# Optimization experiments

Hardware: AMD Instinct MI355X
Metric: run time of the kernel (lower is better)

## Reference

```python
import jax, jax.numpy as jnp
import numpy as np

NUM_HEADS = 16
SIGMA_DATA = 1.0


def setup_inputs() -> dict:
    key = jax.random.key(0)
    ks = jax.random.split(key, 6)
    B, N, C = 4, 2048, 1024
    x = jax.random.normal(ks[0], (B, N, C), dtype=jnp.float32)
    t = jax.random.uniform(ks[1], (B,), dtype=jnp.float32)
    # Linear layers stored as (in, out) so y = x @ W + b
    Wqkv = jax.random.normal(ks[2], (C, 3 * C), dtype=jnp.float32) * (C ** -0.5)
    bqkv = jax.random.normal(ks[3], (3 * C,), dtype=jnp.float32) * 0.02
    Wproj = jax.random.normal(ks[4], (C, C), dtype=jnp.float32) * (C ** -0.5)
    bproj = jax.random.normal(ks[5], (C,), dtype=jnp.float32) * 0.02
    return {"x": x, "t": t, "Wqkv": Wqkv, "bqkv": bqkv, "Wproj": Wproj, "bproj": bproj}


def reference(x, t, Wqkv, bqkv, Wproj, bproj):
    B, N, C = x.shape
    H = NUM_HEADS
    Dh = C // H
    scale = Dh ** -0.5

    qkv = (x @ Wqkv + bqkv).reshape(B, N, 3, H, Dh)
    qkv = jnp.transpose(qkv, (2, 0, 3, 1, 4))
    q, k, v = qkv[0], qkv[1], qkv[2]

    # softmax attention
    scores = jnp.einsum("bhmd,bhnd->bhmn", q, k) * scale
    attn = jax.nn.softmax(scores, axis=-1)
    o = jnp.einsum("bhmn,bhnd->bhmd", attn, v)          # [B, H, N, Dh]
    o = jnp.transpose(o, (0, 2, 1, 3)).reshape(B, N, C)  # [B, N, C]

    # rCM skip coefficients; kernel launch collapses per-batch coeffs to their mean (scalar)
    sd2 = SIGMA_DATA ** 2
    c_skip = (sd2 / (t * t + sd2)).mean()
    c_out = (SIGMA_DATA * t / jnp.sqrt(sd2 + t * t)).mean()

    out = c_skip * x + c_out * o  # fused epilogue
    return out @ Wproj + bproj
```

## Files before the change

### kernel.cpp

```cpp
#include <hip/hip_runtime.h>


typedef unsigned short ushort_t;
typedef __bf16 bf16x8 __attribute__((ext_vector_type(8)));
typedef float f32x4 __attribute__((ext_vector_type(4)));

#define GAS __attribute__((address_space(1)))
#define LAS __attribute__((address_space(3)))

static __device__ __forceinline__ ushort_t f2bf(float f) {
  union { float f; unsigned int u; } v; v.f = f;
  unsigned int r = v.u + 0x7fffu + ((v.u >> 16) & 1u);
  return (ushort_t)(r >> 16);
}

static __device__ __forceinline__ void async16(const void* g, void* l) {
  __builtin_amdgcn_global_load_lds((const GAS unsigned int*)g,
                                   (LAS unsigned int*)l, 16, 0, 0);
}

__global__ __launch_bounds__(256) void prep_kernel(
    const float* __restrict__ x, ushort_t* __restrict__ Xbf,
    const float* __restrict__ Wqkv, ushort_t* __restrict__ WqkvT,
    const float* __restrict__ Wproj, ushort_t* __restrict__ WprojT) {
  __shared__ float tile[32][33];
  const int bid = (int)blockIdx.x, tid = threadIdx.x;
  if (bid < 8192) {
    int i = (bid * 256 + tid) * 4;
    float4 v = *(const float4*)(x + i);
    ushort4 o = make_ushort4(f2bf(v.x), f2bf(v.y), f2bf(v.z), f2bf(v.w));
    *(ushort4*)(Xbf + i) = o;
    return;
  }
  const float* in;
  ushort_t* out;
  int R, C, bx, by;
  if (bid < 11264) {
    int q = bid - 8192;
    by = q / 96; bx = q - by * 96;
    in = Wqkv; out = WqkvT; R = 1024; C = 3072;
  } else {
    int p = bid - 11264;
    bx = p & 31; by = p >> 5;
    in = Wproj; out = WprojT; R = 1024; C = 1024;
  }
  int bc = bx * 32, br = by * 32;
  int tx = tid & 31, ty = tid >> 5;
#pragma unroll
  for (int i = 0; i < 32; i += 8)
    tile[ty + i][tx] = in[(size_t)(br + ty + i) * C + bc + tx];
  __syncthreads();
#pragma unroll
  for (int i = 0; i < 32; i += 8)
    out[(size_t)(bc + ty + i) * R + br + tx] = f2bf(tile[tx][ty + i]);
}

static __device__ __forceinline__ void gemm128_core(
    const ushort_t* __restrict__ A, const ushort_t* __restrict__ Bt, int K,
    int m0, int n0, ushort_t* As, ushort_t* Bs, f32x4 acc[4][4]) {
  const int tid = threadIdx.x;
  const int wave = tid >> 6, lane = tid & 63;
  const int wm = (wave >> 1) * 64, wn = (wave & 1) * 64;
  const int lr = lane & 15, quad = lane >> 4;
  const int ch = ((quad + (lr >> 1)) & 3) * 8;
  for (int kb = 0; kb < K; kb += 32) {
#pragma unroll
    for (int i = 0; i < 2; ++i) {
      int c = (i * 4 + wave) * 64 + lane;
      int row = c >> 2;
      int cg = (((c & 3) - ((c >> 3) & 3)) & 3) * 8;
      async16(A + (size_t)(m0 + row) * K + kb + cg, As + (i * 4 + wave) * 512);
      async16(Bt + (size_t)(n0 + row) * K + kb + cg, Bs + (i * 4 + wave) * 512);
    }
    __syncthreads();
    bf16x8 af[4], bfr[4];
#pragma unroll
    for (int i = 0; i < 4; ++i) {
      af[i]  = *(const bf16x8*)(As + (wm + i * 16 + lr) * 32 + ch);
      bfr[i] = *(const bf16x8*)(Bs + (wn + i * 16 + lr) * 32 + ch);
    }
#pragma unroll
    for (int i = 0; i < 4; ++i)
#pragma unroll
      for (int j = 0; j < 4; ++j)
        acc[i][j] = __builtin_amdgcn_mfma_f32_16x16x32_bf16(af[i], bfr[j], acc[i][j], 0, 0, 0);
    __syncthreads();
  }
}

static __device__ __forceinline__ void grid_decode(int bid, int& m0, int& n0) {
  m0 = (((bid & 7) << 3) | ((bid >> 3) & 7)) << 7;
  n0 = (bid >> 6) << 7;
}

__global__ __launch_bounds__(256) void gemm_qkv_kernel(
    const ushort_t* __restrict__ Xbf, const ushort_t* __restrict__ Wt,
    const float* __restrict__ bqkv, ushort_t* __restrict__ Qb,
    ushort_t* __restrict__ Kb, ushort_t* __restrict__ Vb) {
  __shared__ __align__(16) ushort_t As[128 * 32];
  __shared__ __align__(16) ushort_t Bs[128 * 32];
  int m0, n0;
  grid_decode((int)blockIdx.x, m0, n0);
  f32x4 acc[4][4];
#pragma unroll
  for (int i = 0; i < 4; ++i)
#pragma unroll
    for (int j = 0; j < 4; ++j) acc[i][j] = f32x4{0.f, 0.f, 0.f, 0.f};
  gemm128_core(Xbf, Wt, 1024, m0, n0, As, Bs, acc);

  const int tid = threadIdx.x, wave = tid >> 6, lane = tid & 63;
  const int wm = (wave >> 1) * 64, wn = (wave & 1) * 64;
  const int col = lane & 15, quad = lane >> 4;
  const int b = m0 >> 11;
  const float C1 = 0.18033688011112042f;
#pragma unroll
  for (int j = 0; j < 4; ++j) {
    int jc = n0 + wn + j * 16 + col;
    float bj = bqkv[jc];
    int which = jc >> 10, rem = jc & 1023;
    int hh = rem >> 6, d = rem & 63;
    if (which == 2) {
      size_t vb2 = ((size_t)(b * 16 + hh) * 64 + d) * 2048;
#pragma unroll
      for (int i = 0; i < 4; ++i) {
        int nbase = (m0 + wm + i * 16 + quad * 4) & 2047;
        int npos = (nbase & ~31) | (((nbase >> 2) & 3) << 3) | (((nbase >> 4) & 1) << 2);
        ushort4 pk = make_ushort4(f2bf(acc[i][j][0] + bj), f2bf(acc[i][j][1] + bj),
                                  f2bf(acc[i][j][2] + bj), f2bf(acc[i][j][3] + bj));
        *(ushort4*)(Vb + vb2 + npos) = pk;
      }
    } else {
      ushort_t* dst = which == 0 ? Qb : Kb;
      float sc = which == 0 ? C1 : 1.0f;
      size_t base = ((size_t)(b * 16 + hh) * 2048) * 64 + d;
#pragma unroll
      for (int i = 0; i < 4; ++i)
#pragma unroll
        for (int r = 0; r < 4; ++r) {
          int nseq = (m0 + wm + i * 16 + quad * 4 + r) & 2047;
          dst[base + (size_t)nseq * 64] = f2bf((acc[i][j][r] + bj) * sc);
        }
    }
  }
}

__global__ __launch_bounds__(256) void gemm_out_kernel(
    const ushort_t* __restrict__ Hbf, const ushort_t* __restrict__ Wt,
    const float* __restrict__ bproj, float* __restrict__ out) {
  __shared__ __align__(16) ushort_t As[128 * 32];
  __shared__ __align__(16) ushort_t Bs[128 * 32];
  int m0, n0;
  grid_decode((int)blockIdx.x, m0, n0);
  f32x4 acc[4][4];
#pragma unroll
  for (int i = 0; i < 4; ++i)
#pragma unroll
    for (int j = 0; j < 4; ++j) acc[i][j] = f32x4{0.f, 0.f, 0.f, 0.f};
  gemm128_core(Hbf, Wt, 1024, m0, n0, As, Bs, acc);

  const int tid = threadIdx.x, wave = tid >> 6, lane = tid & 63;
  const int wm = (wave >> 1) * 64, wn = (wave & 1) * 64;
  const int col = lane & 15, quad = lane >> 4;
#pragma unroll
  for (int j = 0; j < 4; ++j) {
    int jc = n0 + wn + j * 16 + col;
    float bj = bproj[jc];
#pragma unroll
    for (int i = 0; i < 4; ++i)
#pragma unroll
      for (int r = 0; r < 4; ++r) {
        int m = m0 + wm + i * 16 + quad * 4 + r;
        out[(size_t)m * 1024 + jc] = acc[i][j][r] + bj;
      }
  }
}

__global__ __launch_bounds__(256, 4) void attn_kernel(
    const ushort_t* __restrict__ Qb, const ushort_t* __restrict__ Kb,
    const ushort_t* __restrict__ Vb, const float* __restrict__ x,
    const float* __restrict__ t, ushort_t* __restrict__ Hbf) {
  __shared__ __align__(16) ushort_t Ks[2][64 * 64];
  __shared__ __align__(16) ushort_t Vs[2][64 * 64];

  const int tid = threadIdx.x, w = tid >> 6, lane = tid & 63;
  const int m = lane & 15, q = lane >> 4;
  const int bid = (int)blockIdx.x;
  const int wg = (bid & 7) * 128 + (bid >> 3);
  const int bh = wg >> 4, rowbase = ((wg & 15) << 7) + w * 32;

  const ushort_t* Qg = Qb + ((size_t)bh * 2048 + rowbase) * 64;
  const ushort_t* Kg = Kb + (size_t)bh * 2048 * 64;
  const ushort_t* Vg = Vb + (size_t)bh * 64 * 2048;

  bf16x8 qf[2][2];
#pragma unroll
  for (int qt = 0; qt < 2; ++qt) {
    qf[qt][0] = *(const bf16x8*)(Qg + (qt * 16 + m) * 64 + q * 8);
    qf[qt][1] = *(const bf16x8*)(Qg + (qt * 16 + m) * 64 + 32 + q * 8);
  }

  auto stage = [&](int kt, int buf) {
#pragma unroll
    for (int i = 0; i < 2; ++i) {
      int f = i * 256 + tid;
      int r = f >> 3, g = (f & 7) ^ (r & 7);
      async16(Kg + (size_t)(kt * 64 + r) * 64 + g * 8,
              Ks[buf] + (size_t)(i * 256 + w * 64) * 8);
    }
#pragma unroll
    for (int i = 0; i < 2; ++i) {
      int f = i * 256 + tid;
      int d = f >> 3, g = (f & 7) ^ (d & 7);
      async16(Vg + (size_t)d * 2048 + kt * 64 + g * 8,
              Vs[buf] + (size_t)(i * 256 + w * 64) * 8);
    }
  };
  stage(0, 0);

  f32x4 oacc[2][4], lacc[2];
#pragma unroll
  for (int qt = 0; qt < 2; ++qt) {
    lacc[qt] = f32x4{0.f, 0.f, 0.f, 0.f};
#pragma unroll
    for (int dt = 0; dt < 4; ++dt) oacc[qt][dt] = f32x4{0.f, 0.f, 0.f, 0.f};
  }

  const float C2 = -23.083120654223414f;
  const f32x4 c2v = {C2, C2, C2, C2};
  const int mk = m & 7;
  union { bf16x8 v; unsigned int u[4]; } onesu;
#pragma unroll
  for (int h = 0; h < 4; ++h) onesu.u[h] = 0x3F803F80u;
  const bf16x8 ones = onesu.v;

#pragma unroll 2
  for (int kt = 0; kt < 32; ++kt) {
    const int cur = kt & 1;
    __syncthreads();
    if (kt < 31) stage(kt + 1, cur ^ 1);
    const ushort_t* K0 = Ks[cur];
    const ushort_t* V0 = Vs[cur];

#pragma unroll
    for (int p = 0; p < 2; ++p) {
      f32x4 st[2][2];
#pragma unroll
      for (int sh = 0; sh < 2; ++sh) {
        int s = p * 2 + sh;
        bf16x8 kf0 = *(const bf16x8*)(K0 + (s * 16 + m) * 64 + (q ^ mk) * 8);
        bf16x8 kf1 = *(const bf16x8*)(K0 + (s * 16 + m) * 64 + ((q + 4) ^ mk) * 8);
#pragma unroll
        for (int qt = 0; qt < 2; ++qt) {
          f32x4 a = __builtin_amdgcn_mfma_f32_16x16x32_bf16(kf0, qf[qt][0], c2v, 0, 0, 0);
          st[sh][qt] = __builtin_amdgcn_mfma_f32_16x16x32_bf16(kf1, qf[qt][1], a, 0, 0, 0);
        }
      }
      bf16x8 pf[2];
#pragma unroll
      for (int qt = 0; qt < 2; ++qt) {
        float pv[8];
#pragma unroll
        for (int sh = 0; sh < 2; ++sh)
#pragma unroll
          for (int rr = 0; rr < 4; ++rr)
            pv[sh * 4 + rr] = __builtin_amdgcn_exp2f(st[sh][qt][rr]);
        union { bf16x8 v; unsigned int u[4]; } pk;
#pragma unroll
        for (int h = 0; h < 4; ++h)
          pk.u[h] = __builtin_amdgcn_perm(__float_as_uint(pv[2 * h + 1]),
                                          __float_as_uint(pv[2 * h]), 0x07060302);
        pf[qt] = pk.v;
      }
#pragma unroll
      for (int dt = 0; dt < 4; ++dt) {
        bf16x8 vf = *(const bf16x8*)(V0 + (dt * 16 + m) * 64 + ((p * 4 + q) ^ mk) * 8);
#pragma unroll
        for (int qt = 0; qt < 2; ++qt)
          oacc[qt][dt] = __builtin_amdgcn_mfma_f32_16x16x32_bf16(vf, pf[qt], oacc[qt][dt], 0, 0, 0);
      }
#pragma unroll
      for (int qt = 0; qt < 2; ++qt)
        lacc[qt] = __builtin_amdgcn_mfma_f32_16x16x32_bf16(ones, pf[qt], lacc[qt], 0, 0, 0);
    }
  }

  float cs = 0.f, co = 0.f;
#pragma unroll
  for (int i = 0; i < 4; ++i) {
    float ti = t[i];
    float d = 1.f + ti * ti;
    cs += 1.f / d;
    co += ti / sqrtf(d);
  }
  cs *= 0.25f; co *= 0.25f;

  const int b = bh >> 4, hh = bh & 15;
#pragma unroll
  for (int qt = 0; qt < 2; ++qt) {
    float inv = co / lacc[qt][0];
    int nseq = rowbase + qt * 16 + m;
#pragma unroll
    for (int dt = 0; dt < 4; ++dt) {
      int c0 = hh * 64 + dt * 16 + q * 4;
      size_t midx = ((size_t)b * 2048 + nseq) * 1024 + c0;
      float4 xv = *(const float4*)(x + midx);
      ushort4 hv = make_ushort4(f2bf(cs * xv.x + oacc[qt][dt][0] * inv),
                                f2bf(cs * xv.y + oacc[qt][dt][1] * inv),
                                f2bf(cs * xv.z + oacc[qt][dt][2] * inv),
                                f2bf(cs * xv.w + oacc[qt][dt][3] * inv));
      *(ushort4*)(Hbf + midx) = hv;
    }
  }
}

extern "C" void kernel_launch(void* const* d_in, const int* in_sizes, int n_in,
                              void* d_out, int out_size, void* d_ws, size_t ws_size,
                              hipStream_t stream) {
  const float* x     = (const float*)d_in[0];
  const float* t     = (const float*)d_in[1];
  const float* Wqkv  = (const float*)d_in[2];
  const float* bqkv  = (const float*)d_in[3];
  const float* Wproj = (const float*)d_in[4];
  const float* bproj = (const float*)d_in[5];
  float* out = (float*)d_out;
  char* ws = (char*)d_ws;

  ushort_t* Xbf    = (ushort_t*)(ws + 256);
  ushort_t* WqkvT  = (ushort_t*)(ws + 256 + 16777216);
  ushort_t* WprojT = (ushort_t*)(ws + 256 + 16777216 + 6291456);
  ushort_t* Qb     = (ushort_t*)(ws + 256 + 16777216 + 6291456 + 2097152);
  ushort_t* Kb = Qb + 8388608;
  ushort_t* Vb = Kb + 8388608;
  ushort_t* Hb = Vb + 8388608;

  prep_kernel<<<12288, 256, 0, stream>>>(x, Xbf, Wqkv, WqkvT, Wproj, WprojT);
  gemm_qkv_kernel<<<1536, 256, 0, stream>>>(Xbf, WqkvT, bqkv, Qb, Kb, Vb);
  attn_kernel<<<1024, 256, 0, stream>>>(Qb, Kb, Vb, x, t, Hb);
  gemm_out_kernel<<<512, 256, 0, stream>>>(Hb, WprojT, bproj, out);
}
```

Before: 263.6 us.

## Double-buffer GEMM core with async LDS prefetch and 64-wide K tiles

Rewrites the shared 128x128 GEMM mainloop to use two LDS buffers, each holding a K-slice of 64 instead of 32. The next tile's global-to-LDS loads are issued while the current tile's MFMAs run, using explicit vmcnt waits and raw barriers in place of two __syncthreads per step. It also switches to an XOR swizzle over 8 chunks to avoid LDS bank conflicts. LDS use per block grows fourfold (to 64 KB), which may reduce occupancy, and the hand-placed waitcnt and barriers add correctness risk.

```diff
diff --git a/kernel.cpp b/kernel.cpp
--- a/kernel.cpp
+++ b/kernel.cpp
@@ -62,29 +62,54 @@
   const int wave = tid >> 6, lane = tid & 63;
   const int wm = (wave >> 1) * 64, wn = (wave & 1) * 64;
   const int lr = lane & 15, quad = lane >> 4;
-  const int ch = ((quad + (lr >> 1)) & 3) * 8;
-  for (int kb = 0; kb < K; kb += 32) {
-#pragma unroll
-    for (int i = 0; i < 2; ++i) {
-      int c = (i * 4 + wave) * 64 + lane;
-      int row = c >> 2;
-      int cg = (((c & 3) - ((c >> 3) & 3)) & 3) * 8;
-      async16(A + (size_t)(m0 + row) * K + kb + cg, As + (i * 4 + wave) * 512);
-      async16(Bt + (size_t)(n0 + row) * K + kb + cg, Bs + (i * 4 + wave) * 512);
-    }
-    __syncthreads();
-    bf16x8 af[4], bfr[4];
-#pragma unroll
-    for (int i = 0; i < 4; ++i) {
-      af[i]  = *(const bf16x8*)(As + (wm + i * 16 + lr) * 32 + ch);
-      bfr[i] = *(const bf16x8*)(Bs + (wn + i * 16 + lr) * 32 + ch);
-    }
+  const int lm = lr & 7;
+
+  auto stage = [&](int kb, int buf) {
+#pragma unroll
+    for (int u = 0; u < 4; ++u) {
+      int f = u * 256 + tid;
+      int r = f >> 3, g = (f & 7) ^ (r & 7);
+      async16(A + (size_t)(m0 + r) * K + kb + g * 8,
+              As + buf * 8192 + (u * 256 + wave * 64) * 8);
+      async16(Bt + (size_t)(n0 + r) * K + kb + g * 8,
+              Bs + buf * 8192 + (u * 256 + wave * 64) * 8);
+    }
+  };
+  stage(0, 0);
+  stage(64, 1);
+
+  const int nt = K >> 6;
+#pragma unroll 2
+  for (int t = 0; t < nt; ++t) {
+    const int cur = t & 1;
+    if (t + 1 < nt) asm volatile("s_waitcnt vmcnt(8)" ::: "memory");
+    else            asm volatile("s_waitcnt vmcnt(0)" ::: "memory");
+    __builtin_amdgcn_s_barrier();
+    __builtin_amdgcn_sched_barrier(0);
+    const ushort_t* As0 = As + cur * 8192;
+    const ushort_t* Bs0 = Bs + cur * 8192;
+    bf16x8 af[4][2], bfr[4][2];
 #pragma unroll
     for (int i = 0; i < 4; ++i)
 #pragma unroll
+      for (int ks = 0; ks < 2; ++ks) {
+        int pos = ((ks * 4 + quad) ^ lm) * 8;
+        af[i][ks]  = *(const bf16x8*)(As0 + (wm + i * 16 + lr) * 64 + pos);
+        bfr[i][ks] = *(const bf16x8*)(Bs0 + (wn + i * 16 + lr) * 64 + pos);
+      }
+    asm volatile("s_waitcnt lgkmcnt(0)" ::: "memory");
+    __builtin_amdgcn_sched_barrier(0);
+    __builtin_amdgcn_s_barrier();
+    __builtin_amdgcn_sched_barrier(0);
+    if (t + 2 < nt) stage((t + 2) << 6, cur);
+#pragma unroll
+    for (int i = 0; i < 4; ++i)
+#pragma unroll
       for (int j = 0; j < 4; ++j)
-        acc[i][j] = __builtin_amdgcn_mfma_f32_16x16x32_bf16(af[i], bfr[j], acc[i][j], 0, 0, 0);
-    __syncthreads();
+#pragma unroll
+        for (int ks = 0; ks < 2; ++ks)
+          acc[i][j] = __builtin_amdgcn_mfma_f32_16x16x32_bf16(af[i][ks], bfr[j][ks],
+                                                              acc[i][j], 0, 0, 0);
   }
 }
 
@@ -97,8 +122,8 @@
     const ushort_t* __restrict__ Xbf, const ushort_t* __restrict__ Wt,
     const float* __restrict__ bqkv, ushort_t* __restrict__ Qb,
     ushort_t* __restrict__ Kb, ushort_t* __restrict__ Vb) {
-  __shared__ __align__(16) ushort_t As[128 * 32];
-  __shared__ __align__(16) ushort_t Bs[128 * 32];
+  __shared__ __align__(16) ushort_t As[2 * 128 * 64];
+  __shared__ __align__(16) ushort_t Bs[2 * 128 * 64];
   int m0, n0;
   grid_decode((int)blockIdx.x, m0, n0);
   f32x4 acc[4][4];
@@ -147,8 +172,8 @@
 __global__ __launch_bounds__(256) void gemm_out_kernel(
     const ushort_t* __restrict__ Hbf, const ushort_t* __restrict__ Wt,
     const float* __restrict__ bproj, float* __restrict__ out) {
-  __shared__ __align__(16) ushort_t As[128 * 32];
-  __shared__ __align__(16) ushort_t Bs[128 * 32];
+  __shared__ __align__(16) ushort_t As[2 * 128 * 64];
+  __shared__ __align__(16) ushort_t Bs[2 * 128 * 64];
   int m0, n0;
   grid_decode((int)blockIdx.x, m0, n0);
   f32x4 acc[4][4];
```

Result: faster. 244.3 us (-7.3%).
